# Optimization experiments

Hardware: AMD Instinct MI355X
Metric: run time of the kernel (lower is better)

The kernel has to match this reference:

```python
import jax, jax.numpy as jnp
import numpy as np

C_IN = 512
C_MID = 256   # in_channels // ratio
ATTN_CH = 32  # SelectiveKernelAttn attn_channels
NUM_PATHS = 2
BN_EPS = 1e-5
LN_EPS = 1e-5


def conv1x1(x, w, b=None):
    # x: [B,C,H,W], w: [O,C] -> [B,O,H,W]
    y = jnp.einsum('oc,bchw->bohw', w, x)
    if b is not None:
        y = y + b[None, :, None, None]
    return y


def setup_inputs() -> dict:
    key = jax.random.key(0)
    ks = jax.random.split(key, 10)
    B, H, W = 16, 64, 64
    s = 0.05
    return {
        'x': jax.random.normal(ks[0], (B, C_IN, H, W), jnp.float32),
        # channel ('ch') branch params
        'w_qr': jax.random.normal(ks[1], (1, C_IN), jnp.float32) * s,
        'b_qr': jnp.zeros((1,), jnp.float32),
        'w_vr': jax.random.normal(ks[2], (C_MID, C_IN), jnp.float32) * s,
        'b_vr': jnp.zeros((C_MID,), jnp.float32),
        'w_up': jax.random.normal(ks[3], (C_IN, C_MID), jnp.float32) * s,
        'b_up': jnp.zeros((C_IN,), jnp.float32),
        'ln_g': jnp.ones((C_IN,), jnp.float32),
        'ln_b': jnp.zeros((C_IN,), jnp.float32),
        # spatial ('sp') branch params
        'w_ql': jax.random.normal(ks[4], (C_MID, C_IN), jnp.float32) * s,
        'b_ql': jnp.zeros((C_MID,), jnp.float32),
        'w_vl': jax.random.normal(ks[5], (C_MID, C_IN), jnp.float32) * s,
        'b_vl': jnp.zeros((C_MID,), jnp.float32),
        # SelectiveKernelAttn params (fc_reduce, bn eval stats, fc_select)
        'w_red': jax.random.normal(ks[6], (ATTN_CH, C_IN), jnp.float32) * s,
        'bn_g': jnp.ones((ATTN_CH,), jnp.float32),
        'bn_b': jnp.zeros((ATTN_CH,), jnp.float32),
        'bn_rm': jnp.zeros((ATTN_CH,), jnp.float32),
        'bn_rv': jnp.ones((ATTN_CH,), jnp.float32),
        'w_sel': jax.random.normal(ks[7], (C_IN * NUM_PATHS, ATTN_CH), jnp.float32) * s,
    }


def reference(x, w_qr, b_qr, w_vr, b_vr, w_up, b_up, ln_g, ln_b,
              w_ql, b_ql, w_vl, b_vl, w_red, bn_g, bn_b, bn_rm, bn_rv, w_sel):
    B, C, H, W = x.shape
    HW = H * W

    # ---- channel attention ('ch') ----
    input_x = conv1x1(x, w_vr, b_vr).reshape(B, C_MID, HW)            # [B,m,HW]
    mask = jax.nn.softmax(conv1x1(x, w_qr, b_qr).reshape(B, HW), axis=1)  # [B,HW]
    context = jnp.einsum('bmh,bh->bm', input_x, mask)                  # [B,m]
    up = jnp.einsum('om,bm->bo', w_up, context) + b_up                 # [B,C]
    mu = jnp.mean(up, axis=1, keepdims=True)
    var = jnp.var(up, axis=1, keepdims=True)
    ln = (up - mu) * jax.lax.rsqrt(var + LN_EPS) * ln_g + ln_b
    channel_attn = jax.nn.sigmoid(ln)                                  # [B,C]

    # ---- spatial attention ('sp') ----
    g_x = conv1x1(x, w_ql, b_ql)                                       # [B,m,H,W]
    avg = jax.nn.softmax(g_x.max(axis=(2, 3)), axis=1)                 # [B,m]
    theta = conv1x1(x, w_vl, b_vl).reshape(B, C_MID, HW)               # [B,m,HW]
    ctx = jnp.einsum('bm,bmh->bh', avg, theta)                         # [B,HW]
    spatial_attn = jax.nn.softmax(ctx, axis=1)                         # [B,HW]

    # ---- dsa fusion ----
    sequence = (channel_attn[:, :, None] * spatial_attn[:, None, :]).reshape(B, C, H, W)
    parallel = (channel_attn[:, :, None] + spatial_attn[:, None, :]).reshape(B, C, H, W)
    stack = jnp.stack([sequence, parallel], axis=1)                    # [B,2,C,H,W]

    # SelectiveKernelAttn (BN in eval mode with running stats)
    s = stack.sum(axis=1).mean(axis=(2, 3))                            # [B,C]
    red = jnp.einsum('ac,bc->ba', w_red, s)                            # [B,attn]
    red = (red - bn_rm) * jax.lax.rsqrt(bn_rv + BN_EPS) * bn_g + bn_b
    red = jax.nn.relu(red)
    sel = jnp.einsum('oa,ba->bo', w_sel, red).reshape(B, NUM_PATHS, C)
    sk_attn = jax.nn.softmax(sel, axis=1)                              # [B,2,C]

    sq_pr = (stack * sk_attn[:, :, :, None, None]).sum(axis=1)         # [B,C,H,W]
    return x * sq_pr + x
```

## Files before the change

kernel.cpp:

```cpp
#include <hip/hip_runtime.h>
#include <hip/hip_bf16.h>

#define BATCH 16
#define CIN   512
#define CMID  256
#define HWN   4096

typedef __bf16 bf16x8  __attribute__((ext_vector_type(8)));
typedef float  floatx4 __attribute__((ext_vector_type(4)));
typedef int    intx4   __attribute__((ext_vector_type(4)));

__device__ __forceinline__ unsigned short f2bf(float f){
  union { float f; unsigned int u; } v; v.f = f;
  unsigned int u = v.u;
  unsigned int r = u + 0x7FFFu + ((u >> 16) & 1u);
  return (unsigned short)(r >> 16);
}

__device__ __forceinline__ float bsum(float v, float* scr, int t){
  #pragma unroll
  for (int o = 32; o >= 1; o >>= 1) v += __shfl_xor(v, o, 64);
  __syncthreads();
  if ((t & 63) == 0) scr[t >> 6] = v;
  __syncthreads();
  return scr[0] + scr[1] + scr[2] + scr[3];
}

__device__ __forceinline__ float bmax(float v, float* scr, int t){
  #pragma unroll
  for (int o = 32; o >= 1; o >>= 1) v = fmaxf(v, __shfl_xor(v, o, 64));
  __syncthreads();
  if ((t & 63) == 0) scr[t >> 6] = v;
  __syncthreads();
  return fmaxf(fmaxf(scr[0], scr[1]), fmaxf(scr[2], scr[3]));
}

__global__ __launch_bounds__(256) void k0_convert(const float* __restrict__ w,
                                                  unsigned short* __restrict__ wbf){
  int i = blockIdx.x * 256 + threadIdx.x;
  wbf[i] = f2bf(w[i]);
}

__global__ __launch_bounds__(256) void k1_gemm(
    const float* __restrict__ x, const unsigned short* __restrict__ wbf,
    const float* __restrict__ w_qr, float* __restrict__ qr, float* __restrict__ gpart)
{
  __shared__ __align__(16) unsigned short Alds[CMID * 32];
  __shared__ __align__(16) unsigned short Blds[64 * 32];
  __shared__ float wqr_s[CIN];

  const int t = threadIdx.x;
  const int ntile = blockIdx.x;
  const int b = blockIdx.y;
  const int n0 = ntile * 64;
  const int lane = t & 63, wave = t >> 6;
  const int grp  = t >> 2;
  const int koff = (t & 3) * 8;

  wqr_s[t] = w_qr[t];
  wqr_s[t + 256] = w_qr[t + 256];

  const float* xb = x + (size_t)b * CIN * HWN;

  floatx4 acc[4][4];
  #pragma unroll
  for (int i = 0; i < 4; ++i)
    #pragma unroll
    for (int j = 0; j < 4; ++j)
      acc[i][j] = (floatx4){0.f, 0.f, 0.f, 0.f};

  float qa = 0.f;
  __syncthreads();

  for (int kt = 0; kt < 16; ++kt){
    const int k0 = kt * 32;
    #pragma unroll
    for (int q = 0; q < 4; ++q){
      const int m = q * 64 + grp;
      *(intx4*)(&Alds[m * 32 + koff]) = *(const intx4*)(&wbf[m * CIN + k0 + koff]);
    }
    float xv[8];
    #pragma unroll
    for (int j = 0; j < 8; ++j)
      xv[j] = xb[(size_t)(k0 + koff + j) * HWN + n0 + grp];
    #pragma unroll
    for (int j = 0; j < 8; ++j)
      qa = fmaf(wqr_s[k0 + koff + j], xv[j], qa);
    union { unsigned short u[8]; intx4 v; } pk;
    #pragma unroll
    for (int j = 0; j < 8; ++j) pk.u[j] = f2bf(xv[j]);
    *(intx4*)(&Blds[grp * 32 + koff]) = pk.v;
    __syncthreads();

    bf16x8 af[4], bfr[4];
    #pragma unroll
    for (int ms = 0; ms < 4; ++ms)
      af[ms]  = *(const bf16x8*)(&Alds[(wave*64 + ms*16 + (lane & 15))*32 + (lane >> 4)*8]);
    #pragma unroll
    for (int ns = 0; ns < 4; ++ns)
      bfr[ns] = *(const bf16x8*)(&Blds[(ns*16 + (lane & 15))*32 + (lane >> 4)*8]);
    #pragma unroll
    for (int ms = 0; ms < 4; ++ms)
      #pragma unroll
      for (int ns = 0; ns < 4; ++ns)
        acc[ms][ns] = __builtin_amdgcn_mfma_f32_16x16x32_bf16(af[ms], bfr[ns], acc[ms][ns], 0, 0, 0);
    __syncthreads();
  }

  qa += __shfl_xor(qa, 1, 64);
  qa += __shfl_xor(qa, 2, 64);
  if ((t & 3) == 0) qr[b * HWN + n0 + grp] = qa;

  #pragma unroll
  for (int ms = 0; ms < 4; ++ms){
    #pragma unroll
    for (int r = 0; r < 4; ++r){
      float v = fmaxf(fmaxf(acc[ms][0][r], acc[ms][1][r]),
                      fmaxf(acc[ms][2][r], acc[ms][3][r]));
      v = fmaxf(v, __shfl_xor(v, 1, 64));
      v = fmaxf(v, __shfl_xor(v, 2, 64));
      v = fmaxf(v, __shfl_xor(v, 4, 64));
      v = fmaxf(v, __shfl_xor(v, 8, 64));
      if ((lane & 15) == 0){
        const int m = wave*64 + ms*16 + (lane >> 4)*4 + r;
        gpart[((b*64 + ntile) * CMID) + m] = v;
      }
    }
  }
}

__global__ __launch_bounds__(256) void k2_small(
    const float* __restrict__ gpart, const float* __restrict__ b_ql,
    const float* __restrict__ w_vl, const float* __restrict__ qr,
    float* __restrict__ wmix, float* __restrict__ stats)
{
  __shared__ float scr[4];
  __shared__ float avg_s[CMID];
  const int b = blockIdx.x, t = threadIdx.x;

  float gm = -3.0e38f;
  for (int nt = 0; nt < 64; ++nt)
    gm = fmaxf(gm, gpart[(b*64 + nt) * CMID + t]);
  gm += b_ql[t];

  float mx = bmax(gm, scr, t);
  float e = expf(gm - mx);
  float s = bsum(e, scr, t);
  avg_s[t] = e / s;
  __syncthreads();

  float w0 = 0.f, w1 = 0.f;
  for (int m = 0; m < CMID; ++m){
    float a = avg_s[m];
    w0 = fmaf(a, w_vl[m*CIN + t], w0);
    w1 = fmaf(a, w_vl[m*CIN + t + 256], w1);
  }
  wmix[b*CIN + t] = w0;
  wmix[b*CIN + t + 256] = w1;

  const float* qb = qr + b*HWN;
  float qm = -3.0e38f;
  for (int i = t; i < HWN; i += 256) qm = fmaxf(qm, qb[i]);
  qm = bmax(qm, scr, t);
  float qs = 0.f;
  for (int i = t; i < HWN; i += 256) qs += expf(qb[i] - qm);
  qs = bsum(qs, scr, t);
  if (t == 0){ stats[b] = qm; stats[16 + b] = qs; }
}

__global__ __launch_bounds__(256) void k3_dual(
    const float* __restrict__ x, const float* __restrict__ qr,
    const float* __restrict__ stats, const float* __restrict__ wmix,
    float* __restrict__ xmask, float* __restrict__ ctx)
{
  const int ht = blockIdx.x, ct = blockIdx.y, b = blockIdx.z;
  const int t = threadIdx.x;
  const int i = t >> 4, j = t & 15;
  const int c0 = ct * 128, h0 = ht * 128;
  const float* xb = x + (size_t)b * CIN * HWN;
  const float qm = stats[b], inv_qs = 1.0f / stats[16 + b];

  float maskv[8], wmv[8];
  #pragma unroll
  for (int l = 0; l < 8; ++l)
    maskv[l] = expf(qr[b*HWN + h0 + j + 16*l] - qm) * inv_qs;
  #pragma unroll
  for (int k = 0; k < 8; ++k)
    wmv[k] = wmix[b*CIN + c0 + i + 16*k];

  float xm[8] = {0,0,0,0,0,0,0,0};
  float cx[8] = {0,0,0,0,0,0,0,0};
  #pragma unroll
  for (int k = 0; k < 8; ++k){
    const float* row = xb + (size_t)(c0 + i + 16*k) * HWN + h0 + j;
    float v[8];
    #pragma unroll
    for (int l = 0; l < 8; ++l) v[l] = row[16*l];
    #pragma unroll
    for (int l = 0; l < 8; ++l){
      xm[k] = fmaf(v[l], maskv[l], xm[k]);
      cx[l] = fmaf(v[l], wmv[k], cx[l]);
    }
  }
  #pragma unroll
  for (int k = 0; k < 8; ++k){
    float v = xm[k];
    v += __shfl_xor(v, 1, 64); v += __shfl_xor(v, 2, 64);
    v += __shfl_xor(v, 4, 64); v += __shfl_xor(v, 8, 64);
    if (j == 0) atomicAdd(&xmask[b*CIN + c0 + i + 16*k], v);
  }
  #pragma unroll
  for (int l = 0; l < 8; ++l){
    float v = cx[l];
    v += __shfl_xor(v, 16, 64); v += __shfl_xor(v, 32, 64);
    if (((t & 63) >> 4) == 0) atomicAdd(&ctx[b*HWN + h0 + j + 16*l], v);
  }
}

__global__ __launch_bounds__(256) void k4_tail(
    const float* __restrict__ xmask, const float* __restrict__ w_vr, const float* __restrict__ b_vr,
    const float* __restrict__ w_up, const float* __restrict__ b_up,
    const float* __restrict__ ln_g, const float* __restrict__ ln_b,
    const float* __restrict__ w_red, const float* __restrict__ bn_g, const float* __restrict__ bn_b,
    const float* __restrict__ bn_rm, const float* __restrict__ bn_rv,
    const float* __restrict__ w_sel, const float* __restrict__ ctxg,
    float* __restrict__ P, float* __restrict__ Q, float* __restrict__ sp)
{
  __shared__ float scr[4];
  __shared__ float xm_s[CIN];
  __shared__ float cm_s[CMID];
  __shared__ float ch_s[CIN];
  __shared__ float red_s[32];
  const int b = blockIdx.x, t = threadIdx.x;

  xm_s[t] = xmask[b*CIN + t];
  xm_s[t + 256] = xmask[b*CIN + t + 256];
  __syncthreads();

  float cacc = b_vr[t];
  const float* wr = w_vr + (size_t)t * CIN;
  for (int c = 0; c < CIN; ++c) cacc = fmaf(wr[c], xm_s[c], cacc);
  cm_s[t] = cacc;
  __syncthreads();

  float up0 = b_up[t], up1 = b_up[t + 256];
  const float* wu0 = w_up + (size_t)t * CMID;
  const float* wu1 = w_up + (size_t)(t + 256) * CMID;
  for (int m = 0; m < CMID; ++m){
    up0 = fmaf(wu0[m], cm_s[m], up0);
    up1 = fmaf(wu1[m], cm_s[m], up1);
  }
  float mu = bsum(up0 + up1, scr, t) * (1.0f / 512.0f);
  float d0 = up0 - mu, d1 = up1 - mu;
  float var = bsum(d0*d0 + d1*d1, scr, t) * (1.0f / 512.0f);
  float rstd = rsqrtf(var + 1e-5f);
  float ch0 = 1.f / (1.f + expf(-(d0 * rstd * ln_g[t] + ln_b[t])));
  float ch1 = 1.f / (1.f + expf(-(d1 * rstd * ln_g[t + 256] + ln_b[t + 256])));
  ch_s[t] = ch0; ch_s[t + 256] = ch1;
  __syncthreads();

  {
    const int a = t >> 3, sub = t & 7;
    float r = 0.f;
    const float* wrd = w_red + a * CIN;
    const float k1 = 1.0f + 1.0f/4096.0f, k2 = 1.0f/4096.0f;
    for (int c = sub; c < CIN; c += 8) r = fmaf(wrd[c], fmaf(ch_s[c], k1, k2), r);
    r += __shfl_xor(r, 1, 64); r += __shfl_xor(r, 2, 64); r += __shfl_xor(r, 4, 64);
    if (sub == 0){
      float bn = (r - bn_rm[a]) * rsqrtf(bn_rv[a] + 1e-5f) * bn_g[a] + bn_b[a];
      red_s[a] = fmaxf(bn, 0.0f);
    }
  }
  __syncthreads();

  #pragma unroll
  for (int q = 0; q < 2; ++q){
    const int c = t + q * 256;
    float s0 = 0.f, s1 = 0.f;
    const float* ws0 = w_sel + (size_t)c * 32;
    const float* ws1 = w_sel + (size_t)(CIN + c) * 32;
    #pragma unroll
    for (int a = 0; a < 32; ++a){
      s0 = fmaf(ws0[a], red_s[a], s0);
      s1 = fmaf(ws1[a], red_s[a], s1);
    }
    float a0 = 1.f / (1.f + expf(s1 - s0));
    float a1 = 1.f - a0;
    float ch = ch_s[c];
    P[b*CIN + c] = 1.0f + a1 * ch;
    Q[b*CIN + c] = a0 * ch + a1;
  }

  const float* cb = ctxg + b * HWN;
  float cm = -3.0e38f;
  for (int h = t; h < HWN; h += 256) cm = fmaxf(cm, cb[h]);
  cm = bmax(cm, scr, t);
  float cs = 0.f;
  for (int h = t; h < HWN; h += 256) cs += expf(cb[h] - cm);
  cs = bsum(cs, scr, t);
  const float inv = 1.0f / cs;
  for (int h = t; h < HWN; h += 256) sp[b*HWN + h] = expf(cb[h] - cm) * inv;
}

__global__ __launch_bounds__(256) void k5_out(
    const float* __restrict__ x, const float* __restrict__ P, const float* __restrict__ Q,
    const float* __restrict__ sp, float* __restrict__ out)
{
  const int bc = blockIdx.x;
  const int b = bc >> 9;
  const int t = threadIdx.x;
  const float p = P[bc], q = Q[bc];
  const floatx4* xr = (const floatx4*)(x + (size_t)bc * HWN);
  const floatx4* sr = (const floatx4*)(sp + (size_t)b * HWN);
  floatx4* outr = (floatx4*)(out + (size_t)bc * HWN);
  #pragma unroll
  for (int r = 0; r < 4; ++r){
    const int idx = t + r * 256;
    floatx4 xv = xr[idx];
    floatx4 sv = sr[idx];
    outr[idx] = xv * (p + sv * q);
  }
}

extern "C" void kernel_launch(void* const* d_in, const int* in_sizes, int n_in,
                              void* d_out, int out_size, void* d_ws, size_t ws_size,
                              hipStream_t stream)
{
  (void)in_sizes; (void)n_in; (void)out_size; (void)ws_size;
  const float* x    = (const float*)d_in[0];
  const float* w_qr = (const float*)d_in[1];
  const float* w_vr = (const float*)d_in[3];
  const float* b_vr = (const float*)d_in[4];
  const float* w_up = (const float*)d_in[5];
  const float* b_up = (const float*)d_in[6];
  const float* ln_g = (const float*)d_in[7];
  const float* ln_b = (const float*)d_in[8];
  const float* w_ql = (const float*)d_in[9];
  const float* b_ql = (const float*)d_in[10];
  const float* w_vl = (const float*)d_in[11];
  const float* w_red = (const float*)d_in[13];
  const float* bn_g  = (const float*)d_in[14];
  const float* bn_b  = (const float*)d_in[15];
  const float* bn_rm = (const float*)d_in[16];
  const float* bn_rv = (const float*)d_in[17];
  const float* w_sel = (const float*)d_in[18];
  float* out = (float*)d_out;

  char* ws = (char*)d_ws;
  unsigned short* wbf = (unsigned short*)(ws + 0);
  float* qr    = (float*)(ws + 262144);
  float* gpart = (float*)(ws + 524288);
  float* wmix  = (float*)(ws + 1572864);
  float* xmask = (float*)(ws + 1605632);
  float* ctx   = (float*)(ws + 1638400);
  float* sp    = (float*)(ws + 1900544);
  float* P     = (float*)(ws + 2162688);
  float* Q     = (float*)(ws + 2195456);
  float* stats = (float*)(ws + 2228224);

  hipMemsetAsync(ws + 1605632, 0, 32768 + 262144, stream);

  k0_convert<<<512, 256, 0, stream>>>(w_ql, wbf);
  k1_gemm<<<dim3(64, BATCH), 256, 0, stream>>>(x, wbf, w_qr, qr, gpart);
  k2_small<<<BATCH, 256, 0, stream>>>(gpart, b_ql, w_vl, qr, wmix, stats);
  k3_dual<<<dim3(32, 4, BATCH), 256, 0, stream>>>(x, qr, stats, wmix, xmask, ctx);
  k4_tail<<<BATCH, 256, 0, stream>>>(xmask, w_vr, b_vr, w_up, b_up, ln_g, ln_b,
                                     w_red, bn_g, bn_b, bn_rm, bn_rv, w_sel, ctx,
                                     P, Q, sp);
  k5_out<<<BATCH * CIN, 256, 0, stream>>>(x, P, Q, sp, out);
}
```

Before: 438.9 us.

## Double-buffer GEMM B tile, load A fragments from global, vectorize dual reduction loads

The GEMM kernel drops the LDS staging of the bf16 weight tile. Each wave now reads its A fragments straight from global memory into registers and prefetches the next k-step's x and weights while the current MFMAs run. The x tile goes into a double-buffered, XOR-swizzled LDS buffer, which lets each k-iteration use one barrier and aims to cut bank conflicts. The dual-reduction kernel switches to float4 row loads, giving each thread four contiguous columns instead of strided scalars. The trade-off is more register pressure and redundant global weight reads across blocks, which rely on the cache.

```diff
diff --git a/kernel.cpp b/kernel.cpp
--- a/kernel.cpp
+++ b/kernel.cpp
@@ -45,71 +45,87 @@
     const float* __restrict__ x, const unsigned short* __restrict__ wbf,
     const float* __restrict__ w_qr, float* __restrict__ qr, float* __restrict__ gpart)
 {
-  __shared__ __align__(16) unsigned short Alds[CMID * 32];
-  __shared__ __align__(16) unsigned short Blds[64 * 32];
+  __shared__ __align__(16) unsigned short Blds[2][64 * 32];
   __shared__ float wqr_s[CIN];
 
   const int t = threadIdx.x;
-  const int ntile = blockIdx.x;
-  const int b = blockIdx.y;
+  const int ntile = blockIdx.x, b = blockIdx.y;
   const int n0 = ntile * 64;
-  const int lane = t & 63, wave = t >> 6;
-  const int grp  = t >> 2;
-  const int koff = (t & 3) * 8;
+  const int lane = t & 63, wave = t >> 6, quad = lane >> 4, lm = lane & 15;
+  const int n_own = t >> 2, q_own = t & 3;
+  const int wblk = (n_own * 4 + (q_own ^ (n_own & 3))) * 8;
 
   wqr_s[t] = w_qr[t];
   wqr_s[t + 256] = w_qr[t + 256];
-
-  const float* xb = x + (size_t)b * CIN * HWN;
+  __syncthreads();
+
+  const float* xb = x + (size_t)b * CIN * HWN + (size_t)(q_own * 8) * HWN + n0 + n_own;
 
   floatx4 acc[4][4];
   #pragma unroll
   for (int i = 0; i < 4; ++i)
     #pragma unroll
-    for (int j = 0; j < 4; ++j)
-      acc[i][j] = (floatx4){0.f, 0.f, 0.f, 0.f};
+    for (int jj = 0; jj < 4; ++jj)
+      acc[i][jj] = (floatx4){0.f, 0.f, 0.f, 0.f};
 
   float qa = 0.f;
-  __syncthreads();
-
+  float xv[8];
+  bf16x8 afc[4], afn[4];
+
+  #pragma unroll
+  for (int j = 0; j < 8; ++j) xv[j] = xb[(size_t)j * HWN];
+  #pragma unroll
+  for (int j = 0; j < 8; ++j) qa = fmaf(wqr_s[q_own * 8 + j], xv[j], qa);
+  {
+    union { unsigned short u[8]; intx4 v; } pk;
+    #pragma unroll
+    for (int j = 0; j < 8; ++j) pk.u[j] = f2bf(xv[j]);
+    *(intx4*)(&Blds[0][wblk]) = pk.v;
+  }
+  #pragma unroll
+  for (int ms = 0; ms < 4; ++ms)
+    afc[ms] = *(const bf16x8*)(&wbf[(size_t)(wave * 64 + ms * 16 + lm) * CIN + quad * 8]);
+  __syncthreads();
+
+  #pragma unroll 2
   for (int kt = 0; kt < 16; ++kt){
-    const int k0 = kt * 32;
-    #pragma unroll
-    for (int q = 0; q < 4; ++q){
-      const int m = q * 64 + grp;
-      *(intx4*)(&Alds[m * 32 + koff]) = *(const intx4*)(&wbf[m * CIN + k0 + koff]);
-    }
-    float xv[8];
-    #pragma unroll
-    for (int j = 0; j < 8; ++j)
-      xv[j] = xb[(size_t)(k0 + koff + j) * HWN + n0 + grp];
-    #pragma unroll
-    for (int j = 0; j < 8; ++j)
-      qa = fmaf(wqr_s[k0 + koff + j], xv[j], qa);
-    union { unsigned short u[8]; intx4 v; } pk;
-    #pragma unroll
-    for (int j = 0; j < 8; ++j) pk.u[j] = f2bf(xv[j]);
-    *(intx4*)(&Blds[grp * 32 + koff]) = pk.v;
-    __syncthreads();
-
-    bf16x8 af[4], bfr[4];
+    const int cur = kt & 1;
+    if (kt < 15){
+      #pragma unroll
+      for (int j = 0; j < 8; ++j) xv[j] = xb[(size_t)((kt + 1) * 32 + j) * HWN];
+      #pragma unroll
+      for (int ms = 0; ms < 4; ++ms)
+        afn[ms] = *(const bf16x8*)(&wbf[(size_t)(wave * 64 + ms * 16 + lm) * CIN +
+                                        (kt + 1) * 32 + quad * 8]);
+    }
+    bf16x8 bfr[4];
+    #pragma unroll
+    for (int ns = 0; ns < 4; ++ns){
+      const int n = ns * 16 + lm;
+      bfr[ns] = *(const bf16x8*)(&Blds[cur][(n * 4 + (quad ^ (n & 3))) * 8]);
+    }
     #pragma unroll
     for (int ms = 0; ms < 4; ++ms)
-      af[ms]  = *(const bf16x8*)(&Alds[(wave*64 + ms*16 + (lane & 15))*32 + (lane >> 4)*8]);
-    #pragma unroll
-    for (int ns = 0; ns < 4; ++ns)
-      bfr[ns] = *(const bf16x8*)(&Blds[(ns*16 + (lane & 15))*32 + (lane >> 4)*8]);
-    #pragma unroll
-    for (int ms = 0; ms < 4; ++ms)
       #pragma unroll
       for (int ns = 0; ns < 4; ++ns)
-        acc[ms][ns] = __builtin_amdgcn_mfma_f32_16x16x32_bf16(af[ms], bfr[ns], acc[ms][ns], 0, 0, 0);
+        acc[ms][ns] = __builtin_amdgcn_mfma_f32_16x16x32_bf16(afc[ms], bfr[ns], acc[ms][ns], 0, 0, 0);
+    if (kt < 15){
+      #pragma unroll
+      for (int j = 0; j < 8; ++j)
+        qa = fmaf(wqr_s[(kt + 1) * 32 + q_own * 8 + j], xv[j], qa);
+      union { unsigned short u[8]; intx4 v; } pk;
+      #pragma unroll
+      for (int j = 0; j < 8; ++j) pk.u[j] = f2bf(xv[j]);
+      *(intx4*)(&Blds[1 - cur][wblk]) = pk.v;
+      #pragma unroll
+      for (int ms = 0; ms < 4; ++ms) afc[ms] = afn[ms];
+    }
     __syncthreads();
   }
 
   qa += __shfl_xor(qa, 1, 64);
   qa += __shfl_xor(qa, 2, 64);
-  if ((t & 3) == 0) qr[b * HWN + n0 + grp] = qa;
+  if ((t & 3) == 0) qr[b * HWN + n0 + n_own] = qa;
 
   #pragma unroll
   for (int ms = 0; ms < 4; ++ms){
@@ -122,8 +138,8 @@
       v = fmaxf(v, __shfl_xor(v, 4, 64));
       v = fmaxf(v, __shfl_xor(v, 8, 64));
       if ((lane & 15) == 0){
-        const int m = wave*64 + ms*16 + (lane >> 4)*4 + r;
-        gpart[((b*64 + ntile) * CMID) + m] = v;
+        const int m = wave * 64 + ms * 16 + (lane >> 4) * 4 + r;
+        gpart[((b * 64 + ntile) * CMID) + m] = v;
       }
     }
   }
@@ -175,33 +191,39 @@
 {
   const int ht = blockIdx.x, ct = blockIdx.y, b = blockIdx.z;
   const int t = threadIdx.x;
-  const int i = t >> 4, j = t & 15;
+  const int j = t & 15, i = t >> 4;
   const int c0 = ct * 128, h0 = ht * 128;
   const float* xb = x + (size_t)b * CIN * HWN;
   const float qm = stats[b], inv_qs = 1.0f / stats[16 + b];
 
-  float maskv[8], wmv[8];
-  #pragma unroll
-  for (int l = 0; l < 8; ++l)
-    maskv[l] = expf(qr[b*HWN + h0 + j + 16*l] - qm) * inv_qs;
+  floatx4 maskv[2];
+  #pragma unroll
+  for (int l = 0; l < 2; ++l)
+    #pragma unroll
+    for (int d = 0; d < 4; ++d)
+      maskv[l][d] = expf(qr[b*HWN + h0 + j*4 + d + 64*l] - qm) * inv_qs;
+
+  float wmv[8];
   #pragma unroll
   for (int k = 0; k < 8; ++k)
     wmv[k] = wmix[b*CIN + c0 + i + 16*k];
 
   float xm[8] = {0,0,0,0,0,0,0,0};
-  float cx[8] = {0,0,0,0,0,0,0,0};
+  floatx4 cx[2];
+  cx[0] = (floatx4){0.f,0.f,0.f,0.f};
+  cx[1] = (floatx4){0.f,0.f,0.f,0.f};
+
   #pragma unroll
   for (int k = 0; k < 8; ++k){
-    const float* row = xb + (size_t)(c0 + i + 16*k) * HWN + h0 + j;
-    float v[8];
-    #pragma unroll
-    for (int l = 0; l < 8; ++l) v[l] = row[16*l];
-    #pragma unroll
-    for (int l = 0; l < 8; ++l){
-      xm[k] = fmaf(v[l], maskv[l], xm[k]);
-      cx[l] = fmaf(v[l], wmv[k], cx[l]);
-    }
-  }
+    const float* row = xb + (size_t)(c0 + i + 16*k) * HWN + h0 + j*4;
+    floatx4 v0 = *(const floatx4*)(row);
+    floatx4 v1 = *(const floatx4*)(row + 64);
+    floatx4 p = v0 * maskv[0] + v1 * maskv[1];
+    xm[k] = (p[0] + p[1]) + (p[2] + p[3]);
+    cx[0] += v0 * wmv[k];
+    cx[1] += v1 * wmv[k];
+  }
+
   #pragma unroll
   for (int k = 0; k < 8; ++k){
     float v = xm[k];
@@ -210,11 +232,13 @@
     if (j == 0) atomicAdd(&xmask[b*CIN + c0 + i + 16*k], v);
   }
   #pragma unroll
-  for (int l = 0; l < 8; ++l){
-    float v = cx[l];
-    v += __shfl_xor(v, 16, 64); v += __shfl_xor(v, 32, 64);
-    if (((t & 63) >> 4) == 0) atomicAdd(&ctx[b*HWN + h0 + j + 16*l], v);
-  }
+  for (int l = 0; l < 2; ++l)
+    #pragma unroll
+    for (int d = 0; d < 4; ++d){
+      float v = cx[l][d];
+      v += __shfl_xor(v, 16, 64); v += __shfl_xor(v, 32, 64);
+      if (((t & 63) >> 4) == 0) atomicAdd(&ctx[b*HWN + h0 + j*4 + d + 64*l], v);
+    }
 }
 
 __global__ __launch_bounds__(256) void k4_tail(
```

Measured after the change: 442.2 us. About the same (+0.7%).
